# Kernel optimization log

Hardware: AMD Instinct MI355X
Metric: run time of the kernel (lower is better)

The kernel has to match this reference:

```python
import jax, jax.numpy as jnp
import numpy as np

B, IN, H, OUT = 1_000_000, 64, 128, 2


def setup_inputs() -> dict:
    key = jax.random.key(0)
    k1, k2, k3, k4 = jax.random.split(key, 4)
    x = jax.random.normal(k1, (B, IN), dtype=jnp.float32)
    u = jax.random.randint(k2, (B,), 0, 3, dtype=jnp.int64)
    # Xavier-uniform-ish init for weights, zeros for biases (as in the module)
    lim1 = float(np.sqrt(6.0 / (IN + H)))
    W1 = jax.random.uniform(k3, (H, IN), dtype=jnp.float32, minval=-lim1, maxval=lim1)
    b1 = jnp.zeros((H,), dtype=jnp.float32)
    lim2 = float(np.sqrt(6.0 / (H + OUT)))
    Wb = jax.random.uniform(k4, (3, OUT, H), dtype=jnp.float32, minval=-lim2, maxval=lim2)
    bb = jnp.zeros((3, OUT), dtype=jnp.float32)
    return {"x": x, "u": u, "W1": W1, "b1": b1, "Wb": Wb, "bb": bb}


def reference(x, u, W1, b1, Wb, bb):
    # shared trunk: linear + relu  -> [B, H]
    h = jax.nn.relu(x @ W1.T + b1)
    # compute all 3 branch heads in one batched GEMM -> [B, 3, OUT]
    out_all = jnp.einsum("bh,koh->bko", h, Wb) + bb
    # hard routing: select head k = u[b] per row (equivalent to gather->scatter)
    u_idx = u.reshape(-1).astype(jnp.int32)
    out = jnp.take_along_axis(out_all, u_idx[:, None, None], axis=1)[:, 0, :]
    return out
```

## Files before the change

kernel.cpp:

```cpp
#include <hip/hip_runtime.h>
#include <stdint.h>


typedef float f32x4 __attribute__((ext_vector_type(4)));
typedef int   i32x4 __attribute__((ext_vector_type(4)));
typedef short short8 __attribute__((ext_vector_type(8)));
typedef __bf16 bf16x8 __attribute__((ext_vector_type(8)));

#define GLOBAL_AS __attribute__((address_space(1)))
#define LDS_AS    __attribute__((address_space(3)))

static __device__ __forceinline__ f32x4 mfma16(bf16x8 a, bf16x8 b, f32x4 c) {
    return __builtin_amdgcn_mfma_f32_16x16x32_bf16(a, b, c, 0, 0, 0);
}

__global__ __launch_bounds__(256) void coil_fused(
    const float* __restrict__ x,
    const int*   __restrict__ u,
    const float* __restrict__ W1,
    const float* __restrict__ b1,
    const float* __restrict__ Wb,
    const float* __restrict__ bb,
    float* __restrict__ out,
    int nTiles, int nWaves)
{
    __shared__ short w1s[128 * 64];
    __shared__ float b1s[128];
    __shared__ float xrA[4][1024];
    __shared__ float xrB[4][1024];

    const int tid  = threadIdx.x;
    const int lane = tid & 63;
    const int c    = lane & 15;
    const int g    = lane >> 4;
    const int wsl  = tid >> 6;

    for (int qq = tid; qq < 1024; qq += 256) {
        int row = qq >> 3;
        const float* src = W1 + row * 64 + (qq & 7) * 8;
        short8 v;
        #pragma unroll
        for (int j = 0; j < 8; ++j) v[j] = __builtin_bit_cast(short, (__bf16)src[j]);
        int phys = (qq * 16) ^ ((row & 7) << 4);
        *reinterpret_cast<short8*>(reinterpret_cast<char*>(w1s) + phys) = v;
    }
    if (tid < 128) b1s[tid] = b1[tid];

    const int ko = c;
    const bool kvalid = (ko < 6);
    bf16x8 B2[4];
    #pragma unroll
    for (int s = 0; s < 4; ++s) {
        #pragma unroll
        for (int j = 0; j < 8; ++j) {
            int n = 32 * s + ((j >> 2) << 4) + 4 * g + (j & 3);
            B2[s][j] = kvalid ? (__bf16)Wb[ko * 128 + n] : (__bf16)0.0f;
        }
    }
    const float bbr = kvalid ? bb[ko] : 0.0f;
    const int khead = ko >> 1, opos = ko & 1;

    __syncthreads();

    int xoff[4];
    #pragma unroll
    for (int i = 0; i < 4; ++i) {
        int p = i * 1024 + lane * 16;
        xoff[i] = p ^ (((p >> 8) & 7) << 4);
    }

    const int sw  = (c & 7) << 4;
    const int r00 = (c * 256 + g * 32 +   0) ^ sw;
    const int r01 = (c * 256 + g * 32 +  16) ^ sw;
    const int r10 = (c * 256 + g * 32 + 128) ^ sw;
    const int r11 = (c * 256 + g * 32 + 144) ^ sw;

    const char* xb8 = reinterpret_cast<const char*>(x);
    const char* w1b = reinterpret_cast<const char*>(w1s);

    auto stage = [&](float* slot, int tile, i32x4& uv) {
        uv = *reinterpret_cast<const i32x4*>(u + tile * 16 + 4 * g);
        const char* src = xb8 + (size_t)tile * 4096;
        LDS_AS char* dst = (LDS_AS char*)slot;
        __builtin_amdgcn_global_load_lds((const GLOBAL_AS void*)(src + xoff[0]), (LDS_AS void*)(dst +    0), 16, 0, 0);
        __builtin_amdgcn_global_load_lds((const GLOBAL_AS void*)(src + xoff[1]), (LDS_AS void*)(dst + 1024), 16, 0, 0);
        __builtin_amdgcn_global_load_lds((const GLOBAL_AS void*)(src + xoff[2]), (LDS_AS void*)(dst + 2048), 16, 0, 0);
        __builtin_amdgcn_global_load_lds((const GLOBAL_AS void*)(src + xoff[3]), (LDS_AS void*)(dst + 3072), 16, 0, 0);
    };

    auto compute = [&](const float* slot, int tile, i32x4 uv) {
        const char* sb = reinterpret_cast<const char*>(slot);
        f32x4 xa = *reinterpret_cast<const f32x4*>(sb + r00);
        f32x4 xv = *reinterpret_cast<const f32x4*>(sb + r01);
        f32x4 xc = *reinterpret_cast<const f32x4*>(sb + r10);
        f32x4 xd = *reinterpret_cast<const f32x4*>(sb + r11);

        bf16x8 B1a, B1b;
        #pragma unroll
        for (int j = 0; j < 4; ++j) {
            B1a[j]     = (__bf16)xa[j];
            B1a[4 + j] = (__bf16)xv[j];
            B1b[j]     = (__bf16)xc[j];
            B1b[4 + j] = (__bf16)xd[j];
        }

        f32x4 oacc = {0.f, 0.f, 0.f, 0.f};
        #pragma unroll
        for (int s = 0; s < 4; ++s) {
            const int t0 = 2 * s, t1 = 2 * s + 1;
            f32x4 h0 = *reinterpret_cast<const f32x4*>(&b1s[16 * t0 + 4 * g]);
            f32x4 h1 = *reinterpret_cast<const f32x4*>(&b1s[16 * t1 + 4 * g]);
            const int lo0 = (16 * t0 + c) * 128 + 16 * g;
            const int lo1 = (16 * t1 + c) * 128 + 16 * g;
            short8 A00 = *reinterpret_cast<const short8*>(w1b + (lo0 ^ sw));
            short8 A01 = *reinterpret_cast<const short8*>(w1b + ((lo0 + 64) ^ sw));
            short8 A10 = *reinterpret_cast<const short8*>(w1b + (lo1 ^ sw));
            short8 A11 = *reinterpret_cast<const short8*>(w1b + ((lo1 + 64) ^ sw));
            h0 = mfma16(__builtin_bit_cast(bf16x8, A00), B1a, h0);
            h1 = mfma16(__builtin_bit_cast(bf16x8, A10), B1a, h1);
            h0 = mfma16(__builtin_bit_cast(bf16x8, A01), B1b, h0);
            h1 = mfma16(__builtin_bit_cast(bf16x8, A11), B1b, h1);
            bf16x8 A2;
            #pragma unroll
            for (int j = 0; j < 4; ++j) {
                A2[j]     = (__bf16)fmaxf(h0[j], 0.0f);
                A2[4 + j] = (__bf16)fmaxf(h1[j], 0.0f);
            }
            oacc = mfma16(A2, B2[s], oacc);
        }

        const int m0 = tile * 16 + 4 * g;
        if (khead == uv[0]) out[(m0 + 0) * 2 + opos] = oacc[0] + bbr;
        if (khead == uv[1]) out[(m0 + 1) * 2 + opos] = oacc[1] + bbr;
        if (khead == uv[2]) out[(m0 + 2) * 2 + opos] = oacc[2] + bbr;
        if (khead == uv[3]) out[(m0 + 3) * 2 + opos] = oacc[3] + bbr;
    };

    const int w = blockIdx.x * 4 + wsl;
    const int nPairs = nTiles >> 1;
    const int qv = nPairs / nWaves, rm = nPairs % nWaves;
    int p          = w * qv + (w < rm ? w : rm);
    const int pend = p + qv + (w < rm ? 1 : 0);
    if (p >= pend) return;

    float* slotA = &xrA[wsl][0];
    float* slotB = &xrB[wsl][0];
    const int lastT = nTiles - 1;

    i32x4 uvA, uvB;
    stage(slotA, 2 * p,     uvA);
    stage(slotB, 2 * p + 1, uvB);

    for (; p < pend; ++p) {
        const int tA = 2 * p, tB = 2 * p + 1;
        compute(slotA, tA, uvA);
        stage(slotA, (tA + 2 <= lastT) ? tA + 2 : lastT, uvA);
        compute(slotB, tB, uvB);
        stage(slotB, (tB + 2 <= lastT) ? tB + 2 : lastT, uvB);
    }
}

extern "C" void kernel_launch(void* const* d_in, const int* in_sizes, int n_in,
                              void* d_out, int out_size, void* d_ws, size_t ws_size,
                              hipStream_t stream) {
    const float* x  = (const float*)d_in[0];
    const int*   u  = (const int*)d_in[1];
    const float* W1 = (const float*)d_in[2];
    const float* b1 = (const float*)d_in[3];
    const float* Wb = (const float*)d_in[4];
    const float* bb = (const float*)d_in[5];
    float* out = (float*)d_out;

    const int B = in_sizes[1];
    const int nTiles = B / 16;

    int blocks = 768;
    int nWaves = blocks * 4;
    int nPairs = nTiles / 2;
    if (nWaves > nPairs) { blocks = (nPairs + 3) / 4; nWaves = blocks * 4; }

    hipLaunchKernelGGL(coil_fused, dim3(blocks), dim3(256), 0, stream,
                       x, u, W1, b1, Wb, bb, out, nTiles, nWaves);
}
```

Baseline: 60.89 us.

## Merge tile-pair staging into one LDS slot and interleave both tiles' MFMAs

Replaces the two per-wave tile buffers with a single 8 KB slot that holds both tiles of a pair. Each iteration reads the pair's x data from LDS into registers, waits on LDS, and immediately issues the next pair's global-to-LDS loads into the same slot. The two tiles' MFMA chains are then interleaved so their dependent chains can overlap. This aims to hide MFMA and bf16-conversion latency and to issue fewer, larger prefetch batches, at the cost of more live registers and a shorter prefetch window than the old two-buffer scheme.

```diff
diff --git a/kernel.cpp b/kernel.cpp
--- a/kernel.cpp
+++ b/kernel.cpp
@@ -22,12 +22,11 @@
     const float* __restrict__ Wb,
     const float* __restrict__ bb,
     float* __restrict__ out,
-    int nTiles, int nWaves)
+    int nPairs, int nWaves)
 {
     __shared__ short w1s[128 * 64];
     __shared__ float b1s[128];
-    __shared__ float xrA[4][1024];
-    __shared__ float xrB[4][1024];
+    __shared__ float xsl[4][2048];
 
     const int tid  = threadIdx.x;
     const int lane = tid & 63;
@@ -62,9 +61,9 @@
 
     __syncthreads();
 
-    int xoff[4];
+    int xoff[8];
     #pragma unroll
-    for (int i = 0; i < 4; ++i) {
+    for (int i = 0; i < 8; ++i) {
         int p = i * 1024 + lane * 16;
         xoff[i] = p ^ (((p >> 8) & 7) << 4);
     }
@@ -77,86 +76,98 @@
 
     const char* xb8 = reinterpret_cast<const char*>(x);
     const char* w1b = reinterpret_cast<const char*>(w1s);
+    float* slot = &xsl[wsl][0];
+    LDS_AS char* dst = (LDS_AS char*)slot;
+    const char* sb = reinterpret_cast<const char*>(slot);
 
-    auto stage = [&](float* slot, int tile, i32x4& uv) {
-        uv = *reinterpret_cast<const i32x4*>(u + tile * 16 + 4 * g);
-        const char* src = xb8 + (size_t)tile * 4096;
-        LDS_AS char* dst = (LDS_AS char*)slot;
-        __builtin_amdgcn_global_load_lds((const GLOBAL_AS void*)(src + xoff[0]), (LDS_AS void*)(dst +    0), 16, 0, 0);
-        __builtin_amdgcn_global_load_lds((const GLOBAL_AS void*)(src + xoff[1]), (LDS_AS void*)(dst + 1024), 16, 0, 0);
-        __builtin_amdgcn_global_load_lds((const GLOBAL_AS void*)(src + xoff[2]), (LDS_AS void*)(dst + 2048), 16, 0, 0);
-        __builtin_amdgcn_global_load_lds((const GLOBAL_AS void*)(src + xoff[3]), (LDS_AS void*)(dst + 3072), 16, 0, 0);
+    auto stage = [&](int pairIdx, i32x4& uvA, i32x4& uvB) {
+        const int t0 = pairIdx * 2;
+        uvA = *reinterpret_cast<const i32x4*>(u + t0 * 16 + 4 * g);
+        uvB = *reinterpret_cast<const i32x4*>(u + t0 * 16 + 16 + 4 * g);
+        const char* src = xb8 + (size_t)t0 * 4096;
+        #pragma unroll
+        for (int i = 0; i < 8; ++i)
+            __builtin_amdgcn_global_load_lds((const GLOBAL_AS void*)(src + xoff[i]),
+                                             (LDS_AS void*)(dst + i * 1024), 16, 0, 0);
     };
 
-    auto compute = [&](const float* slot, int tile, i32x4 uv) {
-        const char* sb = reinterpret_cast<const char*>(slot);
-        f32x4 xa = *reinterpret_cast<const f32x4*>(sb + r00);
-        f32x4 xv = *reinterpret_cast<const f32x4*>(sb + r01);
-        f32x4 xc = *reinterpret_cast<const f32x4*>(sb + r10);
-        f32x4 xd = *reinterpret_cast<const f32x4*>(sb + r11);
+    const int w = blockIdx.x * 4 + wsl;
+    const int qv = nPairs / nWaves, rm = nPairs % nWaves;
+    int p          = w * qv + (w < rm ? w : rm);
+    const int pend = p + qv + (w < rm ? 1 : 0);
+    if (p >= pend) return;
 
-        bf16x8 B1a, B1b;
+    i32x4 uvA, uvB, nuvA, nuvB;
+    stage(p, uvA, uvB);
+
+    for (; p < pend; ++p) {
+        f32x4 xaA = *reinterpret_cast<const f32x4*>(sb + r00);
+        f32x4 xbA = *reinterpret_cast<const f32x4*>(sb + r01);
+        f32x4 xcA = *reinterpret_cast<const f32x4*>(sb + r10);
+        f32x4 xdA = *reinterpret_cast<const f32x4*>(sb + r11);
+        f32x4 xaB = *reinterpret_cast<const f32x4*>(sb + 4096 + r00);
+        f32x4 xbB = *reinterpret_cast<const f32x4*>(sb + 4096 + r01);
+        f32x4 xcB = *reinterpret_cast<const f32x4*>(sb + 4096 + r10);
+        f32x4 xdB = *reinterpret_cast<const f32x4*>(sb + 4096 + r11);
+
+        asm volatile("s_waitcnt lgkmcnt(0)" ::: "memory");
+
+        stage((p + 1 < pend) ? p + 1 : p, nuvA, nuvB);
+
+        bf16x8 B1aA, B1bA, B1aB, B1bB;
         #pragma unroll
         for (int j = 0; j < 4; ++j) {
-            B1a[j]     = (__bf16)xa[j];
-            B1a[4 + j] = (__bf16)xv[j];
-            B1b[j]     = (__bf16)xc[j];
-            B1b[4 + j] = (__bf16)xd[j];
+            B1aA[j] = (__bf16)xaA[j];  B1aA[4 + j] = (__bf16)xbA[j];
+            B1bA[j] = (__bf16)xcA[j];  B1bA[4 + j] = (__bf16)xdA[j];
+            B1aB[j] = (__bf16)xaB[j];  B1aB[4 + j] = (__bf16)xbB[j];
+            B1bB[j] = (__bf16)xcB[j];  B1bB[4 + j] = (__bf16)xdB[j];
         }
 
-        f32x4 oacc = {0.f, 0.f, 0.f, 0.f};
+        f32x4 oaccA = {0.f, 0.f, 0.f, 0.f};
+        f32x4 oaccB = {0.f, 0.f, 0.f, 0.f};
         #pragma unroll
         for (int s = 0; s < 4; ++s) {
             const int t0 = 2 * s, t1 = 2 * s + 1;
-            f32x4 h0 = *reinterpret_cast<const f32x4*>(&b1s[16 * t0 + 4 * g]);
-            f32x4 h1 = *reinterpret_cast<const f32x4*>(&b1s[16 * t1 + 4 * g]);
+            f32x4 bia0 = *reinterpret_cast<const f32x4*>(&b1s[16 * t0 + 4 * g]);
+            f32x4 bia1 = *reinterpret_cast<const f32x4*>(&b1s[16 * t1 + 4 * g]);
             const int lo0 = (16 * t0 + c) * 128 + 16 * g;
             const int lo1 = (16 * t1 + c) * 128 + 16 * g;
             short8 A00 = *reinterpret_cast<const short8*>(w1b + (lo0 ^ sw));
             short8 A01 = *reinterpret_cast<const short8*>(w1b + ((lo0 + 64) ^ sw));
             short8 A10 = *reinterpret_cast<const short8*>(w1b + (lo1 ^ sw));
             short8 A11 = *reinterpret_cast<const short8*>(w1b + ((lo1 + 64) ^ sw));
-            h0 = mfma16(__builtin_bit_cast(bf16x8, A00), B1a, h0);
-            h1 = mfma16(__builtin_bit_cast(bf16x8, A10), B1a, h1);
-            h0 = mfma16(__builtin_bit_cast(bf16x8, A01), B1b, h0);
-            h1 = mfma16(__builtin_bit_cast(bf16x8, A11), B1b, h1);
-            bf16x8 A2;
+            f32x4 h0A = bia0, h1A = bia1, h0B = bia0, h1B = bia1;
+            h0A = mfma16(__builtin_bit_cast(bf16x8, A00), B1aA, h0A);
+            h0B = mfma16(__builtin_bit_cast(bf16x8, A00), B1aB, h0B);
+            h1A = mfma16(__builtin_bit_cast(bf16x8, A10), B1aA, h1A);
+            h1B = mfma16(__builtin_bit_cast(bf16x8, A10), B1aB, h1B);
+            h0A = mfma16(__builtin_bit_cast(bf16x8, A01), B1bA, h0A);
+            h0B = mfma16(__builtin_bit_cast(bf16x8, A01), B1bB, h0B);
+            h1A = mfma16(__builtin_bit_cast(bf16x8, A11), B1bA, h1A);
+            h1B = mfma16(__builtin_bit_cast(bf16x8, A11), B1bB, h1B);
+            bf16x8 A2A, A2B;
             #pragma unroll
             for (int j = 0; j < 4; ++j) {
-                A2[j]     = (__bf16)fmaxf(h0[j], 0.0f);
-                A2[4 + j] = (__bf16)fmaxf(h1[j], 0.0f);
+                A2A[j]     = (__bf16)fmaxf(h0A[j], 0.0f);
+                A2A[4 + j] = (__bf16)fmaxf(h1A[j], 0.0f);
+                A2B[j]     = (__bf16)fmaxf(h0B[j], 0.0f);
+                A2B[4 + j] = (__bf16)fmaxf(h1B[j], 0.0f);
             }
-            oacc = mfma16(A2, B2[s], oacc);
+            oaccA = mfma16(A2A, B2[s], oaccA);
+            oaccB = mfma16(A2B, B2[s], oaccB);
         }
 
-        const int m0 = tile * 16 + 4 * g;
-        if (khead == uv[0]) out[(m0 + 0) * 2 + opos] = oacc[0] + bbr;
-        if (khead == uv[1]) out[(m0 + 1) * 2 + opos] = oacc[1] + bbr;
-        if (khead == uv[2]) out[(m0 + 2) * 2 + opos] = oacc[2] + bbr;
-        if (khead == uv[3]) out[(m0 + 3) * 2 + opos] = oacc[3] + bbr;
-    };
+        const int m0 = p * 32 + 4 * g;
+        if (khead == uvA[0]) out[(m0 +  0) * 2 + opos] = oaccA[0] + bbr;
+        if (khead == uvA[1]) out[(m0 +  1) * 2 + opos] = oaccA[1] + bbr;
+        if (khead == uvA[2]) out[(m0 +  2) * 2 + opos] = oaccA[2] + bbr;
+        if (khead == uvA[3]) out[(m0 +  3) * 2 + opos] = oaccA[3] + bbr;
+        if (khead == uvB[0]) out[(m0 + 16) * 2 + opos] = oaccB[0] + bbr;
+        if (khead == uvB[1]) out[(m0 + 17) * 2 + opos] = oaccB[1] + bbr;
+        if (khead == uvB[2]) out[(m0 + 18) * 2 + opos] = oaccB[2] + bbr;
+        if (khead == uvB[3]) out[(m0 + 19) * 2 + opos] = oaccB[3] + bbr;
 
-    const int w = blockIdx.x * 4 + wsl;
-    const int nPairs = nTiles >> 1;
-    const int qv = nPairs / nWaves, rm = nPairs % nWaves;
-    int p          = w * qv + (w < rm ? w : rm);
-    const int pend = p + qv + (w < rm ? 1 : 0);
-    if (p >= pend) return;
-
-    float* slotA = &xrA[wsl][0];
-    float* slotB = &xrB[wsl][0];
-    const int lastT = nTiles - 1;
-
-    i32x4 uvA, uvB;
-    stage(slotA, 2 * p,     uvA);
-    stage(slotB, 2 * p + 1, uvB);
-
-    for (; p < pend; ++p) {
-        const int tA = 2 * p, tB = 2 * p + 1;
-        compute(slotA, tA, uvA);
-        stage(slotA, (tA + 2 <= lastT) ? tA + 2 : lastT, uvA);
-        compute(slotB, tB, uvB);
-        stage(slotB, (tB + 2 <= lastT) ? tB + 2 : lastT, uvB);
+        uvA = nuvA; uvB = nuvB;
     }
 }
 
@@ -173,12 +184,12 @@
 
     const int B = in_sizes[1];
     const int nTiles = B / 16;
+    const int nPairs = nTiles / 2;
 
     int blocks = 768;
     int nWaves = blocks * 4;
-    int nPairs = nTiles / 2;
     if (nWaves > nPairs) { blocks = (nPairs + 3) / 4; nWaves = blocks * 4; }
 
     hipLaunchKernelGGL(coil_fused, dim3(blocks), dim3(256), 0, stream,
-                       x, u, W1, b1, Wb, bb, out, nTiles, nWaves);
+                       x, u, W1, b1, Wb, bb, out, nPairs, nWaves);
 }
```

Result: faster. 53.17 us (-12.7%).

## Process four tiles per wave iteration with one 16KB staging slot

Applied to the files above, without the earlier changes.

Each wave now handles 64 rows (four 16-row tiles) per loop iteration. The W1 fragments loaded from LDS are reused across all four tiles, and the weight reads are amortised over more MFMA work. Staging moves from two 4KB double-buffered slots per wave to a single 16KB slot per wave. The next slot's global-to-LDS load is issued right after the current data is pulled into registers. Blocks shrink to 128 threads, so the grid has half as many waves; this lowers parallelism and raises register pressure in exchange for fewer LDS weight reads per row.

```diff
diff --git a/kernel.cpp b/kernel.cpp
--- a/kernel.cpp
+++ b/kernel.cpp
@@ -14,7 +14,7 @@
     return __builtin_amdgcn_mfma_f32_16x16x32_bf16(a, b, c, 0, 0, 0);
 }
 
-__global__ __launch_bounds__(256) void coil_fused(
+__global__ __launch_bounds__(128) void coil_fused(
     const float* __restrict__ x,
     const int*   __restrict__ u,
     const float* __restrict__ W1,
@@ -22,12 +22,11 @@
     const float* __restrict__ Wb,
     const float* __restrict__ bb,
     float* __restrict__ out,
-    int nTiles, int nWaves)
+    int nSlots, int nWaves)
 {
     __shared__ short w1s[128 * 64];
     __shared__ float b1s[128];
-    __shared__ float xrA[4][1024];
-    __shared__ float xrB[4][1024];
+    __shared__ float xsl[2][4096];
 
     const int tid  = threadIdx.x;
     const int lane = tid & 63;
@@ -35,7 +34,7 @@
     const int g    = lane >> 4;
     const int wsl  = tid >> 6;
 
-    for (int qq = tid; qq < 1024; qq += 256) {
+    for (int qq = tid; qq < 1024; qq += 128) {
         int row = qq >> 3;
         const float* src = W1 + row * 64 + (qq & 7) * 8;
         short8 v;
@@ -44,7 +43,7 @@
         int phys = (qq * 16) ^ ((row & 7) << 4);
         *reinterpret_cast<short8*>(reinterpret_cast<char*>(w1s) + phys) = v;
     }
-    if (tid < 128) b1s[tid] = b1[tid];
+    b1s[tid] = b1[tid];
 
     const int ko = c;
     const bool kvalid = (ko < 6);
@@ -62,11 +61,11 @@
 
     __syncthreads();
 
-    int xoff[4];
+    int xoff[16];
     #pragma unroll
-    for (int i = 0; i < 4; ++i) {
-        int p = i * 1024 + lane * 16;
-        xoff[i] = p ^ (((p >> 8) & 7) << 4);
+    for (int i = 0; i < 16; ++i) {
+        int pb = i * 1024 + lane * 16;
+        xoff[i] = pb ^ (((pb >> 8) & 7) << 4);
     }
 
     const int sw  = (c & 7) << 4;
@@ -77,86 +76,98 @@
 
     const char* xb8 = reinterpret_cast<const char*>(x);
     const char* w1b = reinterpret_cast<const char*>(w1s);
+    float* slot = &xsl[wsl][0];
+    LDS_AS char* dst = (LDS_AS char*)slot;
+    const char* sb = reinterpret_cast<const char*>(slot);
 
-    auto stage = [&](float* slot, int tile, i32x4& uv) {
-        uv = *reinterpret_cast<const i32x4*>(u + tile * 16 + 4 * g);
-        const char* src = xb8 + (size_t)tile * 4096;
-        LDS_AS char* dst = (LDS_AS char*)slot;
-        __builtin_amdgcn_global_load_lds((const GLOBAL_AS void*)(src + xoff[0]), (LDS_AS void*)(dst +    0), 16, 0, 0);
-        __builtin_amdgcn_global_load_lds((const GLOBAL_AS void*)(src + xoff[1]), (LDS_AS void*)(dst + 1024), 16, 0, 0);
-        __builtin_amdgcn_global_load_lds((const GLOBAL_AS void*)(src + xoff[2]), (LDS_AS void*)(dst + 2048), 16, 0, 0);
-        __builtin_amdgcn_global_load_lds((const GLOBAL_AS void*)(src + xoff[3]), (LDS_AS void*)(dst + 3072), 16, 0, 0);
+    auto stage = [&](int slotIdx) {
+        const char* src = xb8 + (size_t)slotIdx * 16384;
+        #pragma unroll
+        for (int i = 0; i < 16; ++i)
+            __builtin_amdgcn_global_load_lds((const GLOBAL_AS void*)(src + xoff[i]),
+                                             (LDS_AS void*)(dst + i * 1024), 16, 0, 0);
     };
 
-    auto compute = [&](const float* slot, int tile, i32x4 uv) {
-        const char* sb = reinterpret_cast<const char*>(slot);
-        f32x4 xa = *reinterpret_cast<const f32x4*>(sb + r00);
-        f32x4 xv = *reinterpret_cast<const f32x4*>(sb + r01);
-        f32x4 xc = *reinterpret_cast<const f32x4*>(sb + r10);
-        f32x4 xd = *reinterpret_cast<const f32x4*>(sb + r11);
-
-        bf16x8 B1a, B1b;
-        #pragma unroll
-        for (int j = 0; j < 4; ++j) {
-            B1a[j]     = (__bf16)xa[j];
-            B1a[4 + j] = (__bf16)xv[j];
-            B1b[j]     = (__bf16)xc[j];
-            B1b[4 + j] = (__bf16)xd[j];
-        }
-
-        f32x4 oacc = {0.f, 0.f, 0.f, 0.f};
-        #pragma unroll
-        for (int s = 0; s < 4; ++s) {
-            const int t0 = 2 * s, t1 = 2 * s + 1;
-            f32x4 h0 = *reinterpret_cast<const f32x4*>(&b1s[16 * t0 + 4 * g]);
-            f32x4 h1 = *reinterpret_cast<const f32x4*>(&b1s[16 * t1 + 4 * g]);
-            const int lo0 = (16 * t0 + c) * 128 + 16 * g;
-            const int lo1 = (16 * t1 + c) * 128 + 16 * g;
-            short8 A00 = *reinterpret_cast<const short8*>(w1b + (lo0 ^ sw));
-            short8 A01 = *reinterpret_cast<const short8*>(w1b + ((lo0 + 64) ^ sw));
-            short8 A10 = *reinterpret_cast<const short8*>(w1b + (lo1 ^ sw));
-            short8 A11 = *reinterpret_cast<const short8*>(w1b + ((lo1 + 64) ^ sw));
-            h0 = mfma16(__builtin_bit_cast(bf16x8, A00), B1a, h0);
-            h1 = mfma16(__builtin_bit_cast(bf16x8, A10), B1a, h1);
-            h0 = mfma16(__builtin_bit_cast(bf16x8, A01), B1b, h0);
-            h1 = mfma16(__builtin_bit_cast(bf16x8, A11), B1b, h1);
-            bf16x8 A2;
-            #pragma unroll
-            for (int j = 0; j < 4; ++j) {
-                A2[j]     = (__bf16)fmaxf(h0[j], 0.0f);
-                A2[4 + j] = (__bf16)fmaxf(h1[j], 0.0f);
-            }
-            oacc = mfma16(A2, B2[s], oacc);
-        }
-
-        const int m0 = tile * 16 + 4 * g;
-        if (khead == uv[0]) out[(m0 + 0) * 2 + opos] = oacc[0] + bbr;
-        if (khead == uv[1]) out[(m0 + 1) * 2 + opos] = oacc[1] + bbr;
-        if (khead == uv[2]) out[(m0 + 2) * 2 + opos] = oacc[2] + bbr;
-        if (khead == uv[3]) out[(m0 + 3) * 2 + opos] = oacc[3] + bbr;
-    };
-
-    const int w = blockIdx.x * 4 + wsl;
-    const int nPairs = nTiles >> 1;
-    const int qv = nPairs / nWaves, rm = nPairs % nWaves;
+    const int w = blockIdx.x * 2 + wsl;
+    const int qv = nSlots / nWaves, rm = nSlots % nWaves;
     int p          = w * qv + (w < rm ? w : rm);
     const int pend = p + qv + (w < rm ? 1 : 0);
     if (p >= pend) return;
 
-    float* slotA = &xrA[wsl][0];
-    float* slotB = &xrB[wsl][0];
-    const int lastT = nTiles - 1;
-
-    i32x4 uvA, uvB;
-    stage(slotA, 2 * p,     uvA);
-    stage(slotB, 2 * p + 1, uvB);
+    stage(p);
 
     for (; p < pend; ++p) {
-        const int tA = 2 * p, tB = 2 * p + 1;
-        compute(slotA, tA, uvA);
-        stage(slotA, (tA + 2 <= lastT) ? tA + 2 : lastT, uvA);
-        compute(slotB, tB, uvB);
-        stage(slotB, (tB + 2 <= lastT) ? tB + 2 : lastT, uvB);
+        const int rowbase = p * 64 + 4 * g;
+        i32x4 uv[4];
+        #pragma unroll
+        for (int t = 0; t < 4; ++t)
+            uv[t] = *reinterpret_cast<const i32x4*>(u + rowbase + 16 * t);
+
+        f32x4 xf[4][4];
+        #pragma unroll
+        for (int t = 0; t < 4; ++t) {
+            const char* tb = sb + t * 4096;
+            xf[t][0] = *reinterpret_cast<const f32x4*>(tb + r00);
+            xf[t][1] = *reinterpret_cast<const f32x4*>(tb + r01);
+            xf[t][2] = *reinterpret_cast<const f32x4*>(tb + r10);
+            xf[t][3] = *reinterpret_cast<const f32x4*>(tb + r11);
+        }
+        asm volatile("s_waitcnt lgkmcnt(0)" ::: "memory");
+
+        if (p + 1 < pend) stage(p + 1);
+
+        bf16x8 B1a[4], B1b[4];
+        #pragma unroll
+        for (int t = 0; t < 4; ++t) {
+            #pragma unroll
+            for (int j = 0; j < 4; ++j) {
+                B1a[t][j]     = (__bf16)xf[t][0][j];
+                B1a[t][4 + j] = (__bf16)xf[t][1][j];
+                B1b[t][j]     = (__bf16)xf[t][2][j];
+                B1b[t][4 + j] = (__bf16)xf[t][3][j];
+            }
+        }
+
+        f32x4 oacc[4];
+        #pragma unroll
+        for (int t = 0; t < 4; ++t) oacc[t] = f32x4{0.f, 0.f, 0.f, 0.f};
+
+        #pragma unroll
+        for (int s = 0; s < 4; ++s) {
+            const int t0 = 2 * s, t1 = 2 * s + 1;
+            f32x4 bia0 = *reinterpret_cast<const f32x4*>(&b1s[16 * t0 + 4 * g]);
+            f32x4 bia1 = *reinterpret_cast<const f32x4*>(&b1s[16 * t1 + 4 * g]);
+            const int lo0 = (16 * t0 + c) * 128 + 16 * g;
+            const int lo1 = (16 * t1 + c) * 128 + 16 * g;
+            bf16x8 A00 = __builtin_bit_cast(bf16x8, *reinterpret_cast<const short8*>(w1b + (lo0 ^ sw)));
+            bf16x8 A01 = __builtin_bit_cast(bf16x8, *reinterpret_cast<const short8*>(w1b + ((lo0 + 64) ^ sw)));
+            bf16x8 A10 = __builtin_bit_cast(bf16x8, *reinterpret_cast<const short8*>(w1b + (lo1 ^ sw)));
+            bf16x8 A11 = __builtin_bit_cast(bf16x8, *reinterpret_cast<const short8*>(w1b + ((lo1 + 64) ^ sw)));
+            #pragma unroll
+            for (int t = 0; t < 4; ++t) {
+                f32x4 h0 = bia0, h1 = bia1;
+                h0 = mfma16(A00, B1a[t], h0);
+                h1 = mfma16(A10, B1a[t], h1);
+                h0 = mfma16(A01, B1b[t], h0);
+                h1 = mfma16(A11, B1b[t], h1);
+                bf16x8 A2;
+                #pragma unroll
+                for (int j = 0; j < 4; ++j) {
+                    A2[j]     = (__bf16)fmaxf(h0[j], 0.0f);
+                    A2[4 + j] = (__bf16)fmaxf(h1[j], 0.0f);
+                }
+                oacc[t] = mfma16(A2, B2[s], oacc[t]);
+            }
+        }
+
+        #pragma unroll
+        for (int t = 0; t < 4; ++t) {
+            const int m0 = p * 64 + t * 16 + 4 * g;
+            if (khead == uv[t][0]) out[(m0 + 0) * 2 + opos] = oacc[t][0] + bbr;
+            if (khead == uv[t][1]) out[(m0 + 1) * 2 + opos] = oacc[t][1] + bbr;
+            if (khead == uv[t][2]) out[(m0 + 2) * 2 + opos] = oacc[t][2] + bbr;
+            if (khead == uv[t][3]) out[(m0 + 3) * 2 + opos] = oacc[t][3] + bbr;
+        }
     }
 }
 
@@ -173,12 +184,12 @@
 
     const int B = in_sizes[1];
     const int nTiles = B / 16;
+    const int nSlots = nTiles / 4;
 
     int blocks = 768;
-    int nWaves = blocks * 4;
-    int nPairs = nTiles / 2;
-    if (nWaves > nPairs) { blocks = (nPairs + 3) / 4; nWaves = blocks * 4; }
+    int nWaves = blocks * 2;
+    if (nWaves > nSlots) { blocks = (nSlots + 1) / 2; nWaves = blocks * 2; }
 
-    hipLaunchKernelGGL(coil_fused, dim3(blocks), dim3(256), 0, stream,
-                       x, u, W1, b1, Wb, bb, out, nTiles, nWaves);
+    hipLaunchKernelGGL(coil_fused, dim3(blocks), dim3(128), 0, stream,
+                       x, u, W1, b1, Wb, bb, out, nSlots, nWaves);
 }
```

After: 55.85 us. 1.09x faster.
